# Kernel tuning notes

Hardware: AMD Instinct MI355X
Metric: run time of the kernel (lower is better)

## Reference

```python
import jax, jax.numpy as jnp
import numpy as np

NUM_LAYERS = 4
D_MODEL = 512
N_HEADS = 8
SEQ = 2048
HIDE = 2048


def setup_inputs() -> dict:
    key = jax.random.key(0)
    ks = jax.random.split(key, 18)
    L, D, Hd = NUM_LAYERS, D_MODEL, HIDE
    s = 0.02
    return {
        "x": jax.random.normal(ks[0], (2, SEQ, D), jnp.float32),
        "qw": jax.random.normal(ks[1], (L, D, D), jnp.float32) * s,
        "qb": jax.random.normal(ks[2], (L, D), jnp.float32) * s,
        "kw": jax.random.normal(ks[3], (L, D, D), jnp.float32) * s,
        "kb": jax.random.normal(ks[4], (L, D), jnp.float32) * s,
        "vw": jax.random.normal(ks[5], (L, D, D), jnp.float32) * s,
        "vb": jax.random.normal(ks[6], (L, D), jnp.float32) * s,
        "ow": jax.random.normal(ks[7], (L, D, D), jnp.float32) * s,
        "ob": jax.random.normal(ks[8], (L, D), jnp.float32) * s,
        "w0": jax.random.normal(ks[9], (L, D, Hd), jnp.float32) * s,
        "b0": jax.random.normal(ks[10], (L, Hd), jnp.float32) * s,
        "w1": jax.random.normal(ks[11], (L, D, Hd), jnp.float32) * s,
        "b1": jax.random.normal(ks[12], (L, Hd), jnp.float32) * s,
        "w2": jax.random.normal(ks[13], (L, Hd, D), jnp.float32) * s,
        "b2": jax.random.normal(ks[14], (L, D), jnp.float32) * s,
        "att_norm_w": jax.random.normal(ks[15], (L, D), jnp.float32),
        "ffn_norm_w": jax.random.normal(ks[16], (L, D), jnp.float32),
    }


def _rmsnorm(x, w):
    # w * x / (mean(x^2, -1)^0.5 + 1e-6)  -- eps added OUTSIDE the sqrt, as in source
    return w * x / (jnp.sqrt(jnp.mean(x * x, axis=-1, keepdims=True)) + 1e-6)


def _attention(x, wq, bq, wk, bk, wv, bv, wo, bo, causal):
    B, S, D = x.shape
    H = N_HEADS
    hd = D // H
    q = (x @ wq + bq).reshape(B, S, H, hd).transpose(0, 2, 1, 3)  # BHSd
    k = (x @ wk + bk).reshape(B, S, H, hd).transpose(0, 2, 1, 3)
    v = (x @ wv + bv).reshape(B, S, H, hd).transpose(0, 2, 1, 3)
    scores = jnp.einsum("bhqd,bhkd->bhqk", q, k) / jnp.sqrt(jnp.float32(hd))
    scores = jax.nn.softmax(scores + causal, axis=-1)  # BHSS
    o = jnp.einsum("bhqk,bhkd->bhqd", scores, v)
    o = o.transpose(0, 2, 1, 3).reshape(B, S, D)
    return o @ wo + bo


def reference(x, qw, qb, kw, kb, vw, vb, ow, ob, w0, b0, w1, b1, w2, b2, att_norm_w, ffn_norm_w):
    S = x.shape[1]
    # upper-triangular (excl. diag) additive -inf mask, as in the torch buffer
    causal = jnp.where(jnp.triu(jnp.ones((S, S), bool), k=1), -jnp.inf, 0.0).astype(x.dtype)
    h = x
    for i in range(NUM_LAYERS):
        a = _attention(_rmsnorm(h, att_norm_w[i]), qw[i], qb[i], kw[i], kb[i],
                       vw[i], vb[i], ow[i], ob[i], causal)
        h = a + h
        y = _rmsnorm(h, ffn_norm_w[i])
        y = ((y @ w0[i] + b0[i]) * jax.nn.silu(y @ w1[i] + b1[i])) @ w2[i] + b2[i]
        h = y + h
    return h
```

## Files before the change

### kernel.cpp

```cpp
#include <hip/hip_runtime.h>
#include <math.h>

typedef unsigned int   uint4v __attribute__((ext_vector_type(4)));
typedef float          f32x4  __attribute__((ext_vector_type(4)));
typedef __bf16         bf16x8 __attribute__((ext_vector_type(8)));
typedef unsigned short u16x8  __attribute__((ext_vector_type(8)));
typedef unsigned short u16x4  __attribute__((ext_vector_type(4)));

#define D_MODEL 512
#define SEQ     2048
#define BTOK    4096
#define HIDE    2048
#define NHEAD   8
#define HD      64

static __device__ __forceinline__ unsigned short f2bf(float f) {
  __bf16 b = (__bf16)f;
  return __builtin_bit_cast(unsigned short, b);
}
static __device__ __forceinline__ float bf2f(unsigned short b) {
  union { unsigned u; float f; } v; v.u = ((unsigned)b) << 16;
  return v.f;
}
static __device__ __forceinline__ bf16x8 ldb8(const unsigned short* p) {
  return __builtin_bit_cast(bf16x8, *(const uint4v*)p);
}
static __device__ __forceinline__ f32x4 mfma16(bf16x8 a, bf16x8 b, f32x4 c) {
  return __builtin_amdgcn_mfma_f32_16x16x32_bf16(a, b, c, 0, 0, 0);
}

typedef unsigned int u32_g __attribute__((address_space(1)));
typedef unsigned int u32_l __attribute__((address_space(3)));
static __device__ __forceinline__ void gload16(const unsigned short* g, unsigned short* l) {
  __builtin_amdgcn_global_load_lds((const u32_g*)(const void*)g,
                                   (u32_l*)(void*)l, 16, 0, 0);
}

#define SWZ(r, off) ((off) ^ (((r) & 7) << 4))
#define QSCALE 0.180336880f

__global__ __launch_bounds__(64) void prep_t(
    const float* __restrict__ qw, const float* __restrict__ kw,
    const float* __restrict__ vw, const float* __restrict__ ow,
    const float* __restrict__ w0, const float* __restrict__ w1,
    const float* __restrict__ w2,
    unsigned short* __restrict__ Wq, unsigned short* __restrict__ Wo,
    unsigned short* __restrict__ W01, unsigned short* __restrict__ W2)
{
  int bid = blockIdx.x;
  int l = bid >> 10;
  int r = bid & 1023;
  const float* src; unsigned short* dst;
  int tr, tc, srcN, dstK;
  if (r < 192) {
    int sel = r >> 6, tt = r & 63;
    tr = tt >> 3; tc = tt & 7;
    src = (sel == 0 ? qw : sel == 1 ? kw : vw) + (size_t)l * 262144;
    srcN = 512; dstK = 512;
    dst = Wq + (size_t)l * 786432 + (size_t)(sel * 512 + tc * 64) * 512 + tr * 64;
  } else if (r < 256) {
    int tt = r - 192; tr = tt >> 3; tc = tt & 7;
    src = ow + (size_t)l * 262144; srcN = 512; dstK = 512;
    dst = Wo + (size_t)l * 262144 + (size_t)(tc * 64) * 512 + tr * 64;
  } else if (r < 768) {
    int idx = r - 256; int sel = idx >> 8; int tt = idx & 255;
    tr = tt >> 5; tc = tt & 31;
    src = (sel ? w1 : w0) + (size_t)l * 1048576; srcN = 2048; dstK = 512;
    dst = W01 + (size_t)l * 2097152 + (size_t)sel * 1048576 + (size_t)(tc * 64) * 512 + tr * 64;
  } else {
    int tt = r - 768; tr = tt >> 3; tc = tt & 7;
    src = w2 + (size_t)l * 1048576; srcN = 512; dstK = 2048;
    dst = W2 + (size_t)l * 1048576 + (size_t)(tc * 64) * 2048 + tr * 64;
  }
  src += (size_t)(tr * 64) * srcN + tc * 64;
  __shared__ unsigned short T[64][68];
  int t = threadIdx.x;
  #pragma unroll
  for (int it = 0; it < 16; ++it) {
    int row = it * 4 + (t >> 4);
    int col = (t & 15) * 4;
    f32x4 v4 = *(const f32x4*)(src + (size_t)row * srcN + col);
    u16x4 o; o[0] = f2bf(v4.x); o[1] = f2bf(v4.y); o[2] = f2bf(v4.z); o[3] = f2bf(v4.w);
    *(u16x4*)&T[row][col] = o;
  }
  __syncthreads();
  unsigned short* orow = dst + (size_t)t * dstK;
  #pragma unroll
  for (int j0 = 0; j0 < 8; ++j0) {
    u16x8 o;
    #pragma unroll
    for (int j = 0; j < 8; ++j) o[j] = T[j0 * 8 + j][t];
    *(u16x8*)(orow + j0 * 8) = o;
  }
}

__global__ __launch_bounds__(256) void initrms_k(const float* __restrict__ x,
                                                 const float* __restrict__ w,
                                                 float* __restrict__ h,
                                                 unsigned short* __restrict__ xn) {
  int row  = blockIdx.x * 4 + (threadIdx.x >> 6);
  int lane = threadIdx.x & 63;
  const float* xr = x + (size_t)row * D_MODEL + lane * 8;
  f32x4 v0 = *(const f32x4*)(xr);
  f32x4 v1 = *(const f32x4*)(xr + 4);
  *(f32x4*)(h + (size_t)row * D_MODEL + lane * 8)     = v0;
  *(f32x4*)(h + (size_t)row * D_MODEL + lane * 8 + 4) = v1;
  float ss = v0.x*v0.x + v0.y*v0.y + v0.z*v0.z + v0.w*v0.w
           + v1.x*v1.x + v1.y*v1.y + v1.z*v1.z + v1.w*v1.w;
  #pragma unroll
  for (int m = 1; m < 64; m <<= 1) ss += __shfl_xor(ss, m, 64);
  float inv = 1.0f / (sqrtf(ss * (1.0f / D_MODEL)) + 1e-6f);
  f32x4 w0 = *(const f32x4*)(w + lane * 8);
  f32x4 w1 = *(const f32x4*)(w + lane * 8 + 4);
  u16x8 o;
  o[0] = f2bf(v0.x * w0.x * inv); o[1] = f2bf(v0.y * w0.y * inv);
  o[2] = f2bf(v0.z * w0.z * inv); o[3] = f2bf(v0.w * w0.w * inv);
  o[4] = f2bf(v1.x * w1.x * inv); o[5] = f2bf(v1.y * w1.y * inv);
  o[6] = f2bf(v1.z * w1.z * inv); o[7] = f2bf(v1.w * w1.w * inv);
  *(u16x8*)(xn + (size_t)row * D_MODEL + lane * 8) = o;
}

__global__ __launch_bounds__(256) void addrms_k(float* __restrict__ h,
                                                const unsigned short* __restrict__ y,
                                                const float* __restrict__ w,
                                                unsigned short* __restrict__ xn) {
  int row  = blockIdx.x * 4 + (threadIdx.x >> 6);
  int lane = threadIdx.x & 63;
  float* hr = h + (size_t)row * D_MODEL + lane * 8;
  f32x4 v0 = *(const f32x4*)(hr);
  f32x4 v1 = *(const f32x4*)(hr + 4);
  u16x8 yy = *(const u16x8*)(y + (size_t)row * D_MODEL + lane * 8);
  v0.x += bf2f(yy[0]); v0.y += bf2f(yy[1]); v0.z += bf2f(yy[2]); v0.w += bf2f(yy[3]);
  v1.x += bf2f(yy[4]); v1.y += bf2f(yy[5]); v1.z += bf2f(yy[6]); v1.w += bf2f(yy[7]);
  *(f32x4*)(hr)     = v0;
  *(f32x4*)(hr + 4) = v1;
  float ss = v0.x*v0.x + v0.y*v0.y + v0.z*v0.z + v0.w*v0.w
           + v1.x*v1.x + v1.y*v1.y + v1.z*v1.z + v1.w*v1.w;
  #pragma unroll
  for (int m = 1; m < 64; m <<= 1) ss += __shfl_xor(ss, m, 64);
  float inv = 1.0f / (sqrtf(ss * (1.0f / D_MODEL)) + 1e-6f);
  f32x4 w0 = *(const f32x4*)(w + lane * 8);
  f32x4 w1 = *(const f32x4*)(w + lane * 8 + 4);
  u16x8 o;
  o[0] = f2bf(v0.x * w0.x * inv); o[1] = f2bf(v0.y * w0.y * inv);
  o[2] = f2bf(v0.z * w0.z * inv); o[3] = f2bf(v0.w * w0.w * inv);
  o[4] = f2bf(v1.x * w1.x * inv); o[5] = f2bf(v1.y * w1.y * inv);
  o[6] = f2bf(v1.z * w1.z * inv); o[7] = f2bf(v1.w * w1.w * inv);
  *(u16x8*)(xn + (size_t)row * D_MODEL + lane * 8) = o;
}

#define EPI_QKV   0
#define EPI_PLAIN 1

template<int EPI, int BM, int BN>
__global__ __launch_bounds__(256) void gemm5_k(
    const unsigned short* __restrict__ A,
    const unsigned short* __restrict__ Bt,
    const float* __restrict__ bias0,
    const float* __restrict__ bias1,
    const float* __restrict__ bias2,
    void* __restrict__ out0,
    void* __restrict__ out1,
    void* __restrict__ out2,
    int M, int N, int K)
{
  constexpr int MF = BM / 32;
  constexpr int NF = BN / 32;
  constexpr int ALOADS = BM / 32;
  constexpr int BLOADS = BN / 32;

  __shared__ __attribute__((aligned(16))) unsigned short Al[BM * 64];
  __shared__ __attribute__((aligned(16))) unsigned short Bl[BN * 64];

  int nblk = gridDim.x;
  int orig = blockIdx.x;
  int qq = nblk >> 3, rr = nblk & 7, xcd = orig & 7, pos = orig >> 3;
  int lid = (xcd < rr ? xcd * (qq + 1) : rr * (qq + 1) + (xcd - rr) * qq) + pos;
  int numN = N / BN;
  int mt = lid / numN, nt = lid % numN;
  int m0 = mt * BM, n0 = nt * BN;

  int tid = threadIdx.x, lane = tid & 63, w = tid >> 6;
  int wm = w >> 1, wn = w & 1;
  int g = lane >> 4, c = lane & 15;
  int srow = lane >> 3, sslot = lane & 7;
  int sgc = (sslot ^ srow) * 8;

  const unsigned short* aG = A  + (size_t)(m0 + w * (BM / 4) + srow) * K + sgc;
  const unsigned short* bG = Bt + (size_t)(n0 + w * (BN / 4) + srow) * K + sgc;
  unsigned short* aL = &Al[(w * (BM / 4) + srow) * 64 + sslot * 8];
  unsigned short* bL = &Bl[(w * (BN / 4) + srow) * 64 + sslot * 8];

  f32x4 acc[MF][NF] = {};
  int KT = K >> 6;
  int rk = c & 7;

  for (int kt = 0; kt < KT; ++kt) {
    if (kt) __syncthreads();
    #pragma unroll
    for (int t = 0; t < ALOADS; ++t)
      gload16(aG + (size_t)(t * 8) * K + kt * 64, aL + t * 8 * 64);
    #pragma unroll
    for (int t = 0; t < BLOADS; ++t)
      gload16(bG + (size_t)(t * 8) * K + kt * 64, bL + t * 8 * 64);
    __syncthreads();
    #pragma unroll
    for (int ks = 0; ks < 2; ++ks) {
      int slot = (ks * 4 + g) ^ rk;
      bf16x8 af[MF], bfr[NF];
      #pragma unroll
      for (int i = 0; i < MF; ++i)
        af[i] = ldb8(&Al[(wm * (MF * 16) + i * 16 + c) * 64 + slot * 8]);
      #pragma unroll
      for (int j = 0; j < NF; ++j)
        bfr[j] = ldb8(&Bl[(wn * (NF * 16) + j * 16 + c) * 64 + slot * 8]);
      #pragma unroll
      for (int i = 0; i < MF; ++i)
        #pragma unroll
        for (int j = 0; j < NF; ++j)
          acc[i][j] = mfma16(af[i], bfr[j], acc[i][j]);
    }
  }

  #pragma unroll
  for (int i = 0; i < MF; ++i) {
    int mrow = m0 + wm * (MF * 16) + i * 16 + g * 4;
    #pragma unroll
    for (int j = 0; j < NF; ++j) {
      int n = n0 + wn * (NF * 16) + j * 16 + c;
      if (EPI == EPI_QKV) {
        int sel  = n >> 9;
        int nloc = n & 511;
        const float* bp = sel == 0 ? bias0 : sel == 1 ? bias1 : bias2;
        unsigned short* o = (unsigned short*)(sel == 0 ? out0 : sel == 1 ? out1 : out2);
        float sc = (sel == 0) ? QSCALE : 1.0f;
        float bn = bp[nloc];
        #pragma unroll
        for (int ii = 0; ii < 4; ++ii)
          o[(size_t)(mrow + ii) * D_MODEL + nloc] = f2bf((acc[i][j][ii] + bn) * sc);
      } else {
        float bn = bias0[n];
        unsigned short* o = (unsigned short*)out0;
        #pragma unroll
        for (int ii = 0; ii < 4; ++ii)
          o[(size_t)(mrow + ii) * N + n] = f2bf(acc[i][j][ii] + bn);
      }
    }
  }
}

template<int BM, int BN>
__global__ __launch_bounds__(256) void gemm5d_k(
    const unsigned short* __restrict__ A,
    const unsigned short* __restrict__ B0t,
    const unsigned short* __restrict__ B1t,
    const float* __restrict__ bias0,
    const float* __restrict__ bias1,
    unsigned short* __restrict__ out,
    int M, int N, int K)
{
  constexpr int MF = BM / 32;
  constexpr int NF = BN / 32;
  constexpr int ALOADS = BM / 32;
  constexpr int BLOADS = BN / 32;

  __shared__ __attribute__((aligned(16))) unsigned short Al[BM * 64];
  __shared__ __attribute__((aligned(16))) unsigned short B0l[BN * 64];
  __shared__ __attribute__((aligned(16))) unsigned short B1l[BN * 64];

  int nblk = gridDim.x;
  int orig = blockIdx.x;
  int qq = nblk >> 3, rr = nblk & 7, xcd = orig & 7, pos = orig >> 3;
  int lid = (xcd < rr ? xcd * (qq + 1) : rr * (qq + 1) + (xcd - rr) * qq) + pos;
  int numM = M / BM;
  int nt = lid / numM, mt = lid % numM;
  int m0 = mt * BM, n0 = nt * BN;

  int tid = threadIdx.x, lane = tid & 63, w = tid >> 6;
  int wm = w >> 1, wn = w & 1;
  int g = lane >> 4, c = lane & 15;
  int srow = lane >> 3, sslot = lane & 7;
  int sgc = (sslot ^ srow) * 8;

  const unsigned short* aG  = A   + (size_t)(m0 + w * (BM / 4) + srow) * K + sgc;
  const unsigned short* b0G = B0t + (size_t)(n0 + w * (BN / 4) + srow) * K + sgc;
  const unsigned short* b1G = B1t + (size_t)(n0 + w * (BN / 4) + srow) * K + sgc;
  unsigned short* aL  = &Al [(w * (BM / 4) + srow) * 64 + sslot * 8];
  unsigned short* b0L = &B0l[(w * (BN / 4) + srow) * 64 + sslot * 8];
  unsigned short* b1L = &B1l[(w * (BN / 4) + srow) * 64 + sslot * 8];

  f32x4 acc0[MF][NF] = {};
  f32x4 acc1[MF][NF] = {};
  int KT = K >> 6;
  int rk = c & 7;

  for (int kt = 0; kt < KT; ++kt) {
    if (kt) __syncthreads();
    #pragma unroll
    for (int t = 0; t < ALOADS; ++t)
      gload16(aG + (size_t)(t * 8) * K + kt * 64, aL + t * 8 * 64);
    #pragma unroll
    for (int t = 0; t < BLOADS; ++t) {
      gload16(b0G + (size_t)(t * 8) * K + kt * 64, b0L + t * 8 * 64);
      gload16(b1G + (size_t)(t * 8) * K + kt * 64, b1L + t * 8 * 64);
    }
    __syncthreads();
    #pragma unroll
    for (int ks = 0; ks < 2; ++ks) {
      int slot = (ks * 4 + g) ^ rk;
      bf16x8 af[MF], b0f[NF], b1f[NF];
      #pragma unroll
      for (int i = 0; i < MF; ++i)
        af[i] = ldb8(&Al[(wm * (MF * 16) + i * 16 + c) * 64 + slot * 8]);
      #pragma unroll
      for (int j = 0; j < NF; ++j) {
        b0f[j] = ldb8(&B0l[(wn * (NF * 16) + j * 16 + c) * 64 + slot * 8]);
        b1f[j] = ldb8(&B1l[(wn * (NF * 16) + j * 16 + c) * 64 + slot * 8]);
      }
      #pragma unroll
      for (int i = 0; i < MF; ++i)
        #pragma unroll
        for (int j = 0; j < NF; ++j) {
          acc0[i][j] = mfma16(af[i], b0f[j], acc0[i][j]);
          acc1[i][j] = mfma16(af[i], b1f[j], acc1[i][j]);
        }
    }
  }

  #pragma unroll
  for (int i = 0; i < MF; ++i) {
    int mrow = m0 + wm * (MF * 16) + i * 16 + g * 4;
    #pragma unroll
    for (int j = 0; j < NF; ++j) {
      int n = n0 + wn * (NF * 16) + j * 16 + c;
      float b0n = bias0[n], b1n = bias1[n];
      #pragma unroll
      for (int ii = 0; ii < 4; ++ii) {
        float a  = acc0[i][j][ii] + b0n;
        float gv = acc1[i][j][ii] + b1n;
        float s  = gv / (1.0f + __expf(-gv));
        out[(size_t)(mrow + ii) * N + n] = f2bf(a * s);
      }
    }
  }
}

__global__ __launch_bounds__(64) void vtrans_k(const unsigned short* __restrict__ V,
                                               unsigned short* __restrict__ VT) {
  __shared__ unsigned short T[64][76];
  int t = threadIdx.x;
  int s0 = blockIdx.x * 64;
  int bh = blockIdx.y, b = bh >> 3, h = bh & 7;
  const unsigned short* src = V + (size_t)(b * SEQ + s0) * D_MODEL + h * HD;
  #pragma unroll
  for (int j0 = 0; j0 < 8; ++j0) {
    u16x8 vv = *(const u16x8*)(src + (size_t)t * D_MODEL + j0 * 8);
    *(u16x8*)&T[t][j0 * 8] = vv;
  }
  __syncthreads();
  unsigned short* dst = VT + ((size_t)bh * HD + t) * SEQ + s0;
  #pragma unroll
  for (int j0 = 0; j0 < 8; ++j0) {
    u16x8 o;
    #pragma unroll
    for (int j = 0; j < 8; ++j) o[j] = T[j0 * 8 + j][t];
    *(u16x8*)(dst + j0 * 8) = o;
  }
}

struct Stg { uint4v k0, k1, v0, v1; };

static __device__ __forceinline__ Stg stage_load(const unsigned short* Kp,
                                                 const unsigned short* Vp,
                                                 int kbase, int srow, int sslot) {
  Stg s;
  const unsigned short* kr = Kp + (size_t)(kbase + srow) * D_MODEL + sslot * 8;
  s.k0 = *(const uint4v*)kr;
  s.k1 = *(const uint4v*)(kr + 32);
  const unsigned short* vr = Vp + (size_t)srow * SEQ + kbase + sslot * 8;
  s.v0 = *(const uint4v*)vr;
  s.v1 = *(const uint4v*)(vr + 32);
  return s;
}
static __device__ __forceinline__ void stage_write(unsigned short* Klb, unsigned short* Vlb,
                                                   const Stg& s, int srow, int sslot) {
  char* kb = (char*)Klb;
  *(uint4v*)(kb + SWZ(srow, srow * 128 + sslot * 16))       = s.k0;
  *(uint4v*)(kb + SWZ(srow, srow * 128 + (sslot + 4) * 16)) = s.k1;
  char* vb = (char*)Vlb;
  *(uint4v*)(vb + SWZ(srow, srow * 128 + sslot * 16))       = s.v0;
  *(uint4v*)(vb + SWZ(srow, srow * 128 + (sslot + 4) * 16)) = s.v1;
}

template<bool MASKED>
static __device__ __forceinline__ void attn_tile(
    const unsigned short* Klb, const unsigned short* Vlb,
    bf16x8 qf0, bf16x8 qf1, f32x4* oacc, float& ps,
    int g, int c, int kbase, int qrow)
{
  f32x4 z[4];
  #pragma unroll
  for (int hh = 0; hh < 4; ++hh) {
    int r = hh * 16 + c;
    const char* base = (const char*)Klb;
    bf16x8 k0 = ldb8((const unsigned short*)(base + SWZ(r, r * 128 + g * 16)));
    bf16x8 k1 = ldb8((const unsigned short*)(base + SWZ(r, r * 128 + 64 + g * 16)));
    f32x4 t = {};
    t = mfma16(k0, qf0, t);
    t = mfma16(k1, qf1, t);
    z[hh] = t;
  }
  u16x8 pa0, pa1;
  #pragma unroll
  for (int hh = 0; hh < 4; ++hh) {
    #pragma unroll
    for (int i = 0; i < 4; ++i) {
      float p = exp2f(z[hh][i]);
      if (MASKED && (kbase + hh * 16 + g * 4 + i > qrow)) p = 0.0f;
      ps += p;
      unsigned short pb = f2bf(p);
      if (hh < 2) pa0[hh * 4 + i] = pb;
      else        pa1[(hh - 2) * 4 + i] = pb;
    }
  }
  bf16x8 af0 = __builtin_bit_cast(bf16x8, pa0);
  bf16x8 af1 = __builtin_bit_cast(bf16x8, pa1);
  #pragma unroll
  for (int db = 0; db < 4; ++db) {
    int r = db * 16 + c;
    const char* base = (const char*)Vlb;
    u16x4 v00 = *(const u16x4*)(base + SWZ(r, r * 128 + g * 8));
    u16x4 v01 = *(const u16x4*)(base + SWZ(r, r * 128 + 32 + g * 8));
    u16x4 v10 = *(const u16x4*)(base + SWZ(r, r * 128 + 64 + g * 8));
    u16x4 v11 = *(const u16x4*)(base + SWZ(r, r * 128 + 96 + g * 8));
    u16x8 vb0, vb1;
    #pragma unroll
    for (int j = 0; j < 4; ++j) {
      vb0[j] = v00[j]; vb0[4 + j] = v01[j];
      vb1[j] = v10[j]; vb1[4 + j] = v11[j];
    }
    oacc[db] = mfma16(af0, __builtin_bit_cast(bf16x8, vb0), oacc[db]);
    oacc[db] = mfma16(af1, __builtin_bit_cast(bf16x8, vb1), oacc[db]);
  }
}

static __device__ __forceinline__ int slot_base(int c) {
  if (c < 16) return (c - 8) * 2;
  if (c < 24) return 16 + (c - 16) * 3;
  return 40 + (c - 24) * 4;
}

__global__ __launch_bounds__(256) void attn5_k(const unsigned short* __restrict__ Q,
                                               const unsigned short* __restrict__ K,
                                               const unsigned short* __restrict__ VT,
                                               unsigned short* __restrict__ O,
                                               float* __restrict__ Oparts,
                                               float* __restrict__ Sparts)
{
  __shared__ __attribute__((aligned(16))) unsigned short Kl[2][64 * 64];
  __shared__ __attribute__((aligned(16))) unsigned short Vl[2][64 * 64];
  int tid = threadIdx.x, lane = tid & 63, w = tid >> 6;
  int g = lane >> 4, cl = lane & 15;

  int z = 79 - (int)blockIdx.x;
  int c, sp;
  if (z < 8)        { c = z;                    sp = 0; }
  else if (z < 24)  { int t2 = z - 8;  c = 8  + (t2 >> 1); sp = t2 & 1; }
  else if (z < 48)  { int t2 = z - 24; c = 16 + t2 / 3;    sp = t2 % 3; }
  else              { int t2 = z - 48; c = 24 + (t2 >> 2); sp = t2 & 3; }
  int kt0 = sp * 8;
  int kt1 = min(c + 1, kt0 + 8);
  bool lastsplit = (kt1 == c + 1);

  int bh = blockIdx.y, b = bh >> 3, h = bh & 7;
  int q0 = c * 64;
  const unsigned short* Qp = Q + (size_t)(b * SEQ) * D_MODEL + h * HD;
  const unsigned short* Kp = K + (size_t)(b * SEQ) * D_MODEL + h * HD;
  const unsigned short* Vp = VT + (size_t)bh * HD * SEQ;

  int qrow = q0 + w * 16 + cl;
  bf16x8 qf0 = ldb8(Qp + (size_t)qrow * D_MODEL + g * 8);
  bf16x8 qf1 = ldb8(Qp + (size_t)qrow * D_MODEL + 32 + g * 8);

  f32x4 oacc[4] = {};
  float ps = 0.0f;
  int srow = tid >> 2, sslot = tid & 3;

  Stg s0 = stage_load(Kp, Vp, kt0 * 64, srow, sslot);
  stage_write(&Kl[0][0], &Vl[0][0], s0, srow, sslot);
  __syncthreads();

  int buf = 0;
  for (int kt = kt0; kt < kt1 - 1; ++kt) {
    Stg sn = stage_load(Kp, Vp, (kt + 1) * 64, srow, sslot);
    attn_tile<false>(&Kl[buf][0], &Vl[buf][0], qf0, qf1, oacc, ps, g, cl, 0, 0);
    stage_write(&Kl[buf ^ 1][0], &Vl[buf ^ 1][0], sn, srow, sslot);
    __syncthreads();
    buf ^= 1;
  }
  if (lastsplit)
    attn_tile<true>(&Kl[buf][0], &Vl[buf][0], qf0, qf1, oacc, ps, g, cl,
                    (kt1 - 1) * 64, qrow);
  else
    attn_tile<false>(&Kl[buf][0], &Vl[buf][0], qf0, qf1, oacc, ps, g, cl, 0, 0);

  ps += __shfl_xor(ps, 16, 64);
  ps += __shfl_xor(ps, 32, 64);

  if (c < 8) {
    f32x4 inv;
    #pragma unroll
    for (int i = 0; i < 4; ++i) inv[i] = 1.0f / __shfl(ps, g * 4 + i, 64);
    #pragma unroll
    for (int db = 0; db < 4; ++db)
      #pragma unroll
      for (int i = 0; i < 4; ++i)
        O[(size_t)(b * SEQ + q0 + w * 16 + g * 4 + i) * D_MODEL + h * HD + db * 16 + cl] =
            f2bf(oacc[db][i] * inv[i]);
  } else {
    size_t slot = (size_t)bh * 72 + slot_base(c) + sp;
    float* Op = Oparts + slot * 4096;
    float* Sp = Sparts + slot * 64;
    #pragma unroll
    for (int db = 0; db < 4; ++db)
      #pragma unroll
      for (int i = 0; i < 4; ++i)
        Op[(w * 16 + g * 4 + i) * 64 + db * 16 + cl] = oacc[db][i];
    if (g == 0) Sp[w * 16 + cl] = ps;
  }
}

__global__ __launch_bounds__(256) void attn_comb_k(const float* __restrict__ Oparts,
                                                   const float* __restrict__ Sparts,
                                                   unsigned short* __restrict__ O) {
  int t  = threadIdx.x;
  int c  = 8 + (int)(blockIdx.x % 24);
  int bh = (int)(blockIdx.x / 24);
  int b = bh >> 3, h = bh & 7;
  int ns = (c + 8) >> 3;
  size_t slot = (size_t)bh * 72 + slot_base(c);
  const float* O0 = Oparts + slot * 4096;
  const float* S0 = Sparts + slot * 64;
  int r = t >> 2, d0 = (t & 3) * 16;
  f32x4 a0 = {}, a1 = {}, a2 = {}, a3 = {};
  float s = 0.0f;
  for (int si = 0; si < ns; ++si) {
    const float* o = O0 + si * 4096 + r * 64 + d0;
    a0 += *(const f32x4*)(o);
    a1 += *(const f32x4*)(o + 4);
    a2 += *(const f32x4*)(o + 8);
    a3 += *(const f32x4*)(o + 12);
    s  += S0[si * 64 + r];
  }
  float inv = 1.0f / s;
  u16x8 w0, w1;
  #pragma unroll
  for (int j = 0; j < 4; ++j) {
    w0[j]     = f2bf(a0[j] * inv); w0[4 + j] = f2bf(a1[j] * inv);
    w1[j]     = f2bf(a2[j] * inv); w1[4 + j] = f2bf(a3[j] * inv);
  }
  unsigned short* dst = O + (size_t)(b * SEQ + c * 64 + r) * D_MODEL + h * HD + d0;
  *(u16x8*)(dst)     = w0;
  *(u16x8*)(dst + 8) = w1;
}

extern "C" void kernel_launch(void* const* d_in, const int* in_sizes, int n_in,
                              void* d_out, int out_size, void* d_ws, size_t ws_size,
                              hipStream_t stream) {
  (void)in_sizes; (void)n_in; (void)out_size; (void)ws_size;
  const float* x   = (const float*)d_in[0];
  const float* qw  = (const float*)d_in[1];
  const float* qb  = (const float*)d_in[2];
  const float* kw  = (const float*)d_in[3];
  const float* kbi = (const float*)d_in[4];
  const float* vw  = (const float*)d_in[5];
  const float* vb  = (const float*)d_in[6];
  const float* ow  = (const float*)d_in[7];
  const float* ob  = (const float*)d_in[8];
  const float* w0  = (const float*)d_in[9];
  const float* b0  = (const float*)d_in[10];
  const float* w1  = (const float*)d_in[11];
  const float* b1  = (const float*)d_in[12];
  const float* w2  = (const float*)d_in[13];
  const float* b2  = (const float*)d_in[14];
  const float* anw = (const float*)d_in[15];
  const float* fnw = (const float*)d_in[16];

  char* ws = (char*)d_ws;
  float*          h    = (float*)ws;
  unsigned short* xn   = (unsigned short*)(ws + (8u  << 20));
  unsigned short* q    = (unsigned short*)(ws + (12u << 20));
  unsigned short* k    = (unsigned short*)(ws + (16u << 20));
  unsigned short* v    = (unsigned short*)(ws + (20u << 20));
  unsigned short* vt   = (unsigned short*)(ws + (24u << 20));
  unsigned short* ao   = (unsigned short*)(ws + (28u << 20));
  unsigned short* y    = (unsigned short*)(ws + (32u << 20));
  unsigned short* hbuf = (unsigned short*)(ws + (12u << 20));
  unsigned short* Wq   = (unsigned short*)(ws + (36u << 20));
  unsigned short* Wo   = (unsigned short*)(ws + (42u << 20));
  unsigned short* W01  = (unsigned short*)(ws + (44u << 20));
  unsigned short* W2   = (unsigned short*)(ws + (60u << 20));
  float*          Opar = (float*)(ws + (68u << 20));
  float*          Spar = (float*)(ws + (86u << 20));

  prep_t<<<4096, 64, 0, stream>>>(qw, kw, vw, ow, w0, w1, w2, Wq, Wo, W01, W2);
  initrms_k<<<BTOK / 4, 256, 0, stream>>>(x, anw, h, xn);

  for (int l = 0; l < 4; ++l) {
    size_t bo  = (size_t)l * D_MODEL;
    size_t bho = (size_t)l * HIDE;

    gemm5_k<EPI_QKV, 128, 64><<<768, 256, 0, stream>>>(
        xn, Wq + (size_t)l * 786432, qb + bo, kbi + bo, vb + bo,
        q, k, v, BTOK, 3 * D_MODEL, D_MODEL);
    vtrans_k<<<dim3(32, 16), 64, 0, stream>>>(v, vt);
    attn5_k<<<dim3(80, 16), 256, 0, stream>>>(q, k, vt, ao, Opar, Spar);
    attn_comb_k<<<384, 256, 0, stream>>>(Opar, Spar, ao);
    gemm5_k<EPI_PLAIN, 64, 64><<<512, 256, 0, stream>>>(
        ao, Wo + (size_t)l * 262144, ob + bo, nullptr, nullptr,
        y, nullptr, nullptr, BTOK, D_MODEL, D_MODEL);
    addrms_k<<<BTOK / 4, 256, 0, stream>>>(h, y, fnw + bo, xn);

    gemm5d_k<128, 64><<<1024, 256, 0, stream>>>(
        xn, W01 + (size_t)l * 2097152, W01 + (size_t)l * 2097152 + 1048576,
        b0 + bho, b1 + bho, hbuf, BTOK, HIDE, D_MODEL);
    gemm5_k<EPI_PLAIN, 64, 64><<<512, 256, 0, stream>>>(
        hbuf, W2 + (size_t)l * 1048576, b2 + bo, nullptr, nullptr,
        y, nullptr, nullptr, BTOK, D_MODEL, HIDE);
    addrms_k<<<BTOK / 4, 256, 0, stream>>>(
        h, y, (l < 3 ? anw + bo + D_MODEL : anw), xn);
  }
  hipMemcpyAsync(d_out, h, (size_t)BTOK * D_MODEL * sizeof(float),
                 hipMemcpyDeviceToDevice, stream);
}
```

Measured before the change: 477.2 us.

## Double-buffer GEMM LDS tiles and fuse V transpose into QKV epilogue

The GEMM kernels now use two LDS buffers, so the global-to-LDS loads for the next K tile are issued before the MFMA work on the current tile, with one barrier per iteration instead of two. The QKV GEMM epilogue writes V tiles through LDS directly into the transposed head-major layout, which removes the separate vtrans kernel and the round trip of V through global memory. This doubles LDS use per block, which may lower occupancy. It also depends on the V-section tiles aligning with single heads and batch boundaries.

```diff
diff --git a/kernel.cpp b/kernel.cpp
--- a/kernel.cpp
+++ b/kernel.cpp
@@ -153,7 +153,7 @@
 #define EPI_PLAIN 1
 
 template<int EPI, int BM, int BN>
-__global__ __launch_bounds__(256) void gemm5_k(
+__global__ __launch_bounds__(256) void gemm6_k(
     const unsigned short* __restrict__ A,
     const unsigned short* __restrict__ Bt,
     const float* __restrict__ bias0,
@@ -169,8 +169,8 @@
   constexpr int ALOADS = BM / 32;
   constexpr int BLOADS = BN / 32;
 
-  __shared__ __attribute__((aligned(16))) unsigned short Al[BM * 64];
-  __shared__ __attribute__((aligned(16))) unsigned short Bl[BN * 64];
+  __shared__ __attribute__((aligned(16))) unsigned short Al[2][BM * 64];
+  __shared__ __attribute__((aligned(16))) unsigned short Bl[2][BN * 64];
 
   int nblk = gridDim.x;
   int orig = blockIdx.x;
@@ -188,57 +188,103 @@
 
   const unsigned short* aG = A  + (size_t)(m0 + w * (BM / 4) + srow) * K + sgc;
   const unsigned short* bG = Bt + (size_t)(n0 + w * (BN / 4) + srow) * K + sgc;
-  unsigned short* aL = &Al[(w * (BM / 4) + srow) * 64 + sslot * 8];
-  unsigned short* bL = &Bl[(w * (BN / 4) + srow) * 64 + sslot * 8];
+  int aOff = (w * (BM / 4) + srow) * 64 + sslot * 8;
+  int bOff = (w * (BN / 4) + srow) * 64 + sslot * 8;
 
   f32x4 acc[MF][NF] = {};
   int KT = K >> 6;
   int rk = c & 7;
 
+  #pragma unroll
+  for (int t = 0; t < ALOADS; ++t)
+    gload16(aG + (size_t)(t * 8) * K, &Al[0][aOff + t * 8 * 64]);
+  #pragma unroll
+  for (int t = 0; t < BLOADS; ++t)
+    gload16(bG + (size_t)(t * 8) * K, &Bl[0][bOff + t * 8 * 64]);
+  __syncthreads();
+
   for (int kt = 0; kt < KT; ++kt) {
-    if (kt) __syncthreads();
-    #pragma unroll
-    for (int t = 0; t < ALOADS; ++t)
-      gload16(aG + (size_t)(t * 8) * K + kt * 64, aL + t * 8 * 64);
-    #pragma unroll
-    for (int t = 0; t < BLOADS; ++t)
-      gload16(bG + (size_t)(t * 8) * K + kt * 64, bL + t * 8 * 64);
-    __syncthreads();
+    int cur = kt & 1;
+    if (kt + 1 < KT) {
+      int nb = cur ^ 1;
+      const unsigned short* aGk = aG + (kt + 1) * 64;
+      const unsigned short* bGk = bG + (kt + 1) * 64;
+      #pragma unroll
+      for (int t = 0; t < ALOADS; ++t)
+        gload16(aGk + (size_t)(t * 8) * K, &Al[nb][aOff + t * 8 * 64]);
+      #pragma unroll
+      for (int t = 0; t < BLOADS; ++t)
+        gload16(bGk + (size_t)(t * 8) * K, &Bl[nb][bOff + t * 8 * 64]);
+    }
     #pragma unroll
     for (int ks = 0; ks < 2; ++ks) {
       int slot = (ks * 4 + g) ^ rk;
       bf16x8 af[MF], bfr[NF];
       #pragma unroll
       for (int i = 0; i < MF; ++i)
-        af[i] = ldb8(&Al[(wm * (MF * 16) + i * 16 + c) * 64 + slot * 8]);
+        af[i] = ldb8(&Al[cur][(wm * (MF * 16) + i * 16 + c) * 64 + slot * 8]);
       #pragma unroll
       for (int j = 0; j < NF; ++j)
-        bfr[j] = ldb8(&Bl[(wn * (NF * 16) + j * 16 + c) * 64 + slot * 8]);
+        bfr[j] = ldb8(&Bl[cur][(wn * (NF * 16) + j * 16 + c) * 64 + slot * 8]);
       #pragma unroll
       for (int i = 0; i < MF; ++i)
         #pragma unroll
         for (int j = 0; j < NF; ++j)
           acc[i][j] = mfma16(af[i], bfr[j], acc[i][j]);
     }
-  }
-
-  #pragma unroll
-  for (int i = 0; i < MF; ++i) {
-    int mrow = m0 + wm * (MF * 16) + i * 16 + g * 4;
-    #pragma unroll
-    for (int j = 0; j < NF; ++j) {
-      int n = n0 + wn * (NF * 16) + j * 16 + c;
-      if (EPI == EPI_QKV) {
-        int sel  = n >> 9;
-        int nloc = n & 511;
-        const float* bp = sel == 0 ? bias0 : sel == 1 ? bias1 : bias2;
-        unsigned short* o = (unsigned short*)(sel == 0 ? out0 : sel == 1 ? out1 : out2);
-        float sc = (sel == 0) ? QSCALE : 1.0f;
-        float bn = bp[nloc];
+    __syncthreads();
+  }
+
+  if (EPI == EPI_QKV) {
+    int sel  = n0 >> 9;
+    if (sel < 2) {
+      #pragma unroll
+      for (int i = 0; i < MF; ++i) {
+        int mrow = m0 + wm * (MF * 16) + i * 16 + g * 4;
         #pragma unroll
-        for (int ii = 0; ii < 4; ++ii)
-          o[(size_t)(mrow + ii) * D_MODEL + nloc] = f2bf((acc[i][j][ii] + bn) * sc);
-      } else {
+        for (int j = 0; j < NF; ++j) {
+          int nloc = (n0 & 511) + wn * (NF * 16) + j * 16 + c;
+          const float* bp = sel == 0 ? bias0 : bias1;
+          unsigned short* o = (unsigned short*)(sel == 0 ? out0 : out1);
+          float sc = (sel == 0) ? QSCALE : 1.0f;
+          float bn = bp[nloc];
+          #pragma unroll
+          for (int ii = 0; ii < 4; ++ii)
+            o[(size_t)(mrow + ii) * D_MODEL + nloc] = f2bf((acc[i][j][ii] + bn) * sc);
+        }
+      }
+    } else {
+      unsigned short* T = &Al[0][0];
+      #pragma unroll
+      for (int i = 0; i < MF; ++i) {
+        int ml0 = wm * (MF * 16) + i * 16 + g * 4;
+        #pragma unroll
+        for (int j = 0; j < NF; ++j) {
+          int nl = wn * (NF * 16) + j * 16 + c;
+          float bn = bias2[(n0 & 511) + nl];
+          u16x4 pk;
+          #pragma unroll
+          for (int ii = 0; ii < 4; ++ii) pk[ii] = f2bf(acc[i][j][ii] + bn);
+          *(u16x4*)&T[nl * 136 + ml0] = pk;
+        }
+      }
+      __syncthreads();
+      int b  = m0 >> 11, s0 = m0 & 2047;
+      int hh = (n0 & 511) >> 6;
+      int r  = tid >> 2, c0 = (tid & 3) * 32;
+      unsigned short* dst = (unsigned short*)out2 +
+          ((size_t)(b * NHEAD + hh) * HD + r) * SEQ + s0 + c0;
+      #pragma unroll
+      for (int u = 0; u < 4; ++u)
+        *(u16x8*)(dst + u * 8) = *(u16x8*)&T[r * 136 + c0 + u * 8];
+    }
+  } else {
+    #pragma unroll
+    for (int i = 0; i < MF; ++i) {
+      int mrow = m0 + wm * (MF * 16) + i * 16 + g * 4;
+      #pragma unroll
+      for (int j = 0; j < NF; ++j) {
+        int n = n0 + wn * (NF * 16) + j * 16 + c;
         float bn = bias0[n];
         unsigned short* o = (unsigned short*)out0;
         #pragma unroll
@@ -250,7 +296,7 @@
 }
 
 template<int BM, int BN>
-__global__ __launch_bounds__(256) void gemm5d_k(
+__global__ __launch_bounds__(256) void gemm6d_k(
     const unsigned short* __restrict__ A,
     const unsigned short* __restrict__ B0t,
     const unsigned short* __restrict__ B1t,
@@ -264,9 +310,9 @@
   constexpr int ALOADS = BM / 32;
   constexpr int BLOADS = BN / 32;
 
-  __shared__ __attribute__((aligned(16))) unsigned short Al[BM * 64];
-  __shared__ __attribute__((aligned(16))) unsigned short B0l[BN * 64];
-  __shared__ __attribute__((aligned(16))) unsigned short B1l[BN * 64];
+  __shared__ __attribute__((aligned(16))) unsigned short Al[2][BM * 64];
+  __shared__ __attribute__((aligned(16))) unsigned short B0l[2][BN * 64];
+  __shared__ __attribute__((aligned(16))) unsigned short B1l[2][BN * 64];
 
   int nblk = gridDim.x;
   int orig = blockIdx.x;
@@ -285,37 +331,51 @@
   const unsigned short* aG  = A   + (size_t)(m0 + w * (BM / 4) + srow) * K + sgc;
   const unsigned short* b0G = B0t + (size_t)(n0 + w * (BN / 4) + srow) * K + sgc;
   const unsigned short* b1G = B1t + (size_t)(n0 + w * (BN / 4) + srow) * K + sgc;
-  unsigned short* aL  = &Al [(w * (BM / 4) + srow) * 64 + sslot * 8];
-  unsigned short* b0L = &B0l[(w * (BN / 4) + srow) * 64 + sslot * 8];
-  unsigned short* b1L = &B1l[(w * (BN / 4) + srow) * 64 + sslot * 8];
+  int aOff = (w * (BM / 4) + srow) * 64 + sslot * 8;
+  int bOff = (w * (BN / 4) + srow) * 64 + sslot * 8;
 
   f32x4 acc0[MF][NF] = {};
   f32x4 acc1[MF][NF] = {};
   int KT = K >> 6;
   int rk = c & 7;
 
+  #pragma unroll
+  for (int t = 0; t < ALOADS; ++t)
+    gload16(aG + (size_t)(t * 8) * K, &Al[0][aOff + t * 8 * 64]);
+  #pragma unroll
+  for (int t = 0; t < BLOADS; ++t) {
+    gload16(b0G + (size_t)(t * 8) * K, &B0l[0][bOff + t * 8 * 64]);
+    gload16(b1G + (size_t)(t * 8) * K, &B1l[0][bOff + t * 8 * 64]);
+  }
+  __syncthreads();
+
   for (int kt = 0; kt < KT; ++kt) {
-    if (kt) __syncthreads();
-    #pragma unroll
-    for (int t = 0; t < ALOADS; ++t)
-      gload16(aG + (size_t)(t * 8) * K + kt * 64, aL + t * 8 * 64);
-    #pragma unroll
-    for (int t = 0; t < BLOADS; ++t) {
-      gload16(b0G + (size_t)(t * 8) * K + kt * 64, b0L + t * 8 * 64);
-      gload16(b1G + (size_t)(t * 8) * K + kt * 64, b1L + t * 8 * 64);
-    }
-    __syncthreads();
+    int cur = kt & 1;
+    if (kt + 1 < KT) {
+      int nb = cur ^ 1;
+      const unsigned short* aGk  = aG  + (kt + 1) * 64;
+      const unsigned short* b0Gk = b0G + (kt + 1) * 64;
+      const unsigned short* b1Gk = b1G + (kt + 1) * 64;
+      #pragma unroll
+      for (int t = 0; t < ALOADS; ++t)
+        gload16(aGk + (size_t)(t * 8) * K, &Al[nb][aOff + t * 8 * 64]);
+      #pragma unroll
+      for (int t = 0; t < BLOADS; ++t) {
+        gload16(b0Gk + (size_t)(t * 8) * K, &B0l[nb][bOff + t * 8 * 64]);
+        gload16(b1Gk + (size_t)(t * 8) * K, &B1l[nb][bOff + t * 8 * 64]);
+      }
+    }
     #pragma unroll
     for (int ks = 0; ks < 2; ++ks) {
       int slot = (ks * 4 + g) ^ rk;
       bf16x8 af[MF], b0f[NF], b1f[NF];
       #pragma unroll
       for (int i = 0; i < MF; ++i)
-        af[i] = ldb8(&Al[(wm * (MF * 16) + i * 16 + c) * 64 + slot * 8]);
+        af[i] = ldb8(&Al[cur][(wm * (MF * 16) + i * 16 + c) * 64 + slot * 8]);
       #pragma unroll
       for (int j = 0; j < NF; ++j) {
-        b0f[j] = ldb8(&B0l[(wn * (NF * 16) + j * 16 + c) * 64 + slot * 8]);
-        b1f[j] = ldb8(&B1l[(wn * (NF * 16) + j * 16 + c) * 64 + slot * 8]);
+        b0f[j] = ldb8(&B0l[cur][(wn * (NF * 16) + j * 16 + c) * 64 + slot * 8]);
+        b1f[j] = ldb8(&B1l[cur][(wn * (NF * 16) + j * 16 + c) * 64 + slot * 8]);
       }
       #pragma unroll
       for (int i = 0; i < MF; ++i)
@@ -325,6 +385,7 @@
           acc1[i][j] = mfma16(af[i], b1f[j], acc1[i][j]);
         }
     }
+    __syncthreads();
   }
 
   #pragma unroll
@@ -342,29 +403,6 @@
         out[(size_t)(mrow + ii) * N + n] = f2bf(a * s);
       }
     }
-  }
-}
-
-__global__ __launch_bounds__(64) void vtrans_k(const unsigned short* __restrict__ V,
-                                               unsigned short* __restrict__ VT) {
-  __shared__ unsigned short T[64][76];
-  int t = threadIdx.x;
-  int s0 = blockIdx.x * 64;
-  int bh = blockIdx.y, b = bh >> 3, h = bh & 7;
-  const unsigned short* src = V + (size_t)(b * SEQ + s0) * D_MODEL + h * HD;
-  #pragma unroll
-  for (int j0 = 0; j0 < 8; ++j0) {
-    u16x8 vv = *(const u16x8*)(src + (size_t)t * D_MODEL + j0 * 8);
-    *(u16x8*)&T[t][j0 * 8] = vv;
-  }
-  __syncthreads();
-  unsigned short* dst = VT + ((size_t)bh * HD + t) * SEQ + s0;
-  #pragma unroll
-  for (int j0 = 0; j0 < 8; ++j0) {
-    u16x8 o;
-    #pragma unroll
-    for (int j = 0; j < 8; ++j) o[j] = T[j0 * 8 + j][t];
-    *(u16x8*)(dst + j0 * 8) = o;
   }
 }
 
@@ -591,7 +629,6 @@
   unsigned short* xn   = (unsigned short*)(ws + (8u  << 20));
   unsigned short* q    = (unsigned short*)(ws + (12u << 20));
   unsigned short* k    = (unsigned short*)(ws + (16u << 20));
-  unsigned short* v    = (unsigned short*)(ws + (20u << 20));
   unsigned short* vt   = (unsigned short*)(ws + (24u << 20));
   unsigned short* ao   = (unsigned short*)(ws + (28u << 20));
   unsigned short* y    = (unsigned short*)(ws + (32u << 20));
@@ -610,21 +647,20 @@
     size_t bo  = (size_t)l * D_MODEL;
     size_t bho = (size_t)l * HIDE;
 
-    gemm5_k<EPI_QKV, 128, 64><<<768, 256, 0, stream>>>(
+    gemm6_k<EPI_QKV, 128, 64><<<768, 256, 0, stream>>>(
         xn, Wq + (size_t)l * 786432, qb + bo, kbi + bo, vb + bo,
-        q, k, v, BTOK, 3 * D_MODEL, D_MODEL);
-    vtrans_k<<<dim3(32, 16), 64, 0, stream>>>(v, vt);
+        q, k, vt, BTOK, 3 * D_MODEL, D_MODEL);
     attn5_k<<<dim3(80, 16), 256, 0, stream>>>(q, k, vt, ao, Opar, Spar);
     attn_comb_k<<<384, 256, 0, stream>>>(Opar, Spar, ao);
-    gemm5_k<EPI_PLAIN, 64, 64><<<512, 256, 0, stream>>>(
+    gemm6_k<EPI_PLAIN, 64, 64><<<512, 256, 0, stream>>>(
         ao, Wo + (size_t)l * 262144, ob + bo, nullptr, nullptr,
         y, nullptr, nullptr, BTOK, D_MODEL, D_MODEL);
     addrms_k<<<BTOK / 4, 256, 0, stream>>>(h, y, fnw + bo, xn);
 
-    gemm5d_k<128, 64><<<1024, 256, 0, stream>>>(
+    gemm6d_k<128, 64><<<1024, 256, 0, stream>>>(
         xn, W01 + (size_t)l * 2097152, W01 + (size_t)l * 2097152 + 1048576,
         b0 + bho, b1 + bho, hbuf, BTOK, HIDE, D_MODEL);
-    gemm5_k<EPI_PLAIN, 64, 64><<<512, 256, 0, stream>>>(
+    gemm6_k<EPI_PLAIN, 64, 64><<<512, 256, 0, stream>>>(
         hbuf, W2 + (size_t)l * 1048576, b2 + bo, nullptr, nullptr,
         y, nullptr, nullptr, BTOK, D_MODEL, HIDE);
     addrms_k<<<BTOK / 4, 256, 0, stream>>>(
```

Result: no change. 471.4 us (-1.2%).
